# Kernel optimization log

Measured on AMD Instinct MI355X. Metric: run time of the kernel, lower is better.

Reference implementation:

```python
import jax, jax.numpy as jnp
import numpy as np

K = 9  # kernel size == stride, asserted by the module


def setup_inputs() -> dict:
    key = jax.random.key(0)
    k1, k2, k3 = jax.random.split(key, 3)
    x = jax.random.normal(k1, (4, 16, 8192), dtype=jnp.float32)
    W = jax.random.normal(k2, (16, 16, K), dtype=jnp.float32) * 0.1  # conv1d weight [out,in,K]
    b = jax.random.normal(k3, (16,), dtype=jnp.float32) * 0.1       # conv1d bias [out]
    return {"x": x, "W": W, "b": b}


def reference(x, W, b):
    # x: [B, C, N]; sampling_type='all', similarity='Col', aggregation='Col',
    # magnitude='euclidean', no shuffle, no padding, no coordinate encoding.
    B, C, N = x.shape
    # squared euclidean distance matrix [B, N, N]
    ns = jnp.sum(x * x, axis=1)                      # [B, N]
    dot = jnp.einsum('bcn,bcm->bnm', x, x)           # [B, N, N]
    dist = jnp.maximum(ns[:, :, None] + ns[:, None, :] - 2.0 * dot, 0.0)
    # diagonal filled with -0.1 so each token is its own nearest neighbor
    eye = jnp.eye(N, dtype=bool)
    dist = jnp.where(eye[None, :, :], jnp.float32(-0.1), dist)
    # euclidean -> maximum=False -> take K smallest distances
    _, idx = jax.lax.top_k(-dist, K)                 # idx: [B, N, K]
    # gather neighbor features: prime[b, :, n, k] = x[b, :, idx[b, n, k]]
    neigh = jax.vmap(lambda xb, ib: xb[:, ib])(x, idx)   # [B, C, N, K]
    # Conv1d(kernel=K, stride=K, padding=0) over the flattened [B, C, N*K] prime
    # tensor == per-token contraction over (C, K)
    out = jnp.einsum('bcnk,ock->bon', neigh, W) + b[None, :, None]  # [B, out, N]
    return out
```

## Files before the change

### kernel.cpp

```cpp
#include <hip/hip_runtime.h>
#include <hip/hip_bf16.h>
#include <math.h>

#define NB 4
#define NC 16
#define NN 8192
#define NK 9
#define CANDN 128
#define MR (NN / 4)
#define HPAD 129

typedef short s16x8 __attribute__((ext_vector_type(8)));
typedef float f32x4 __attribute__((ext_vector_type(4)));

#define OFF_XS   2097152u
#define OFF_NS   4194304u
#define OFF_NK   4325376u
#define OFF_NBR  4456448u
#define OFF_FLAG 5046272u
#define OFF_CAND 5177344u

__global__ void prep_kernel(const float* __restrict__ x,
                            float* __restrict__ xt,
                            float* __restrict__ ns32,
                            float* __restrict__ nk,
                            unsigned short* __restrict__ xs) {
    int t = blockIdx.x * 256 + threadIdx.x;
    int b = t >> 13, m = t & (NN - 1);
    const float* xb = x + (size_t)b * NC * NN;
    float v[NC];
#pragma unroll
    for (int c = 0; c < NC; ++c) v[c] = xb[(size_t)c * NN + m];
    float s = __fmul_rn(v[0], v[0]);
#pragma unroll
    for (int c = 1; c < NC; ++c) s = __fadd_rn(s, __fmul_rn(v[c], v[c]));
    float* o = xt + (size_t)t * NC;
#pragma unroll
    for (int c = 0; c < NC; ++c) o[c] = v[c];
    ns32[t] = s;
    nk[t] = 128.0f + 0.5f * s;
    unsigned short* xo = xs + (size_t)t * 32;
#pragma unroll
    for (int c = 0; c < NC; ++c) {
        __hip_bfloat16 h = __float2bfloat16(v[c]);
        float hf = __bfloat162float(h);
        __hip_bfloat16 l = __float2bfloat16(v[c] - hf);
        xo[c] = *(unsigned short*)&h;
        xo[16 + c] = *(unsigned short*)&l;
    }
}

__device__ __forceinline__ s16x8 negbf(s16x8 v) {
    s16x8 r;
#pragma unroll
    for (int i = 0; i < 8; ++i) r[i] = (short)(v[i] ^ (short)0x8000);
    return r;
}

__global__ __launch_bounds__(256, 4) void topk_kernel(
        const unsigned short* __restrict__ xs, const float* __restrict__ nk,
        unsigned short* __restrict__ cand, unsigned* __restrict__ flags) {
    __shared__ __align__(16) unsigned hist[32 * HPAD];
    __shared__ __align__(16) unsigned short list[32][CANDN];
    __shared__ unsigned cnt[32];
    __shared__ unsigned Bbin[32];
    const int tid = threadIdx.x;
    const int L = tid & 63;
    const int q = tid >> 6;
    const int b = blockIdx.x >> 8;
    const int n0 = (blockIdx.x & 255) * 32;
    const int lrow = L & 15;
    const int lk = L >> 4;

    {
        for (int i = tid; i < 32 * HPAD; i += 256) hist[i] = 0u;
        unsigned* lp = (unsigned*)&list[0][0];
        for (int i = tid; i < 32 * CANDN / 2; i += 256) lp[i] = 0xFFFFFFFFu;
        if (tid < 32) { cnt[tid] = 0u; Bbin[tid] = 127u; }
    }
    __syncthreads();

    const char* xsb = (const char*)xs + (size_t)b * NN * 64;
    const float* nkb = nk + (size_t)b * NN;
    const char* nkc = (const char*)nkb;

    const int khalf = (lk & 1) * 16;
    const int r0 = n0 + lrow, r1 = n0 + 16 + lrow;
    const s16x8 bhi0 = negbf(*(const s16x8*)(xsb + (size_t)r0 * 64 + khalf));
    const s16x8 blo0 = negbf(*(const s16x8*)(xsb + (size_t)r0 * 64 + 32 + khalf));
    const s16x8 bhi1 = negbf(*(const s16x8*)(xsb + (size_t)r1 * 64 + khalf));
    const s16x8 blo1 = negbf(*(const s16x8*)(xsb + (size_t)r1 * 64 + 32 + khalf));

    const float base8_0 = 8.0f * (256.0f - nkb[r0]);
    const float base8_1 = 8.0f * (256.0f - nkb[r1]);

    const int m0 = q * MR;
    const int voffA0 = (m0 + lrow) * 64 + lk * 16;
    const int voffK0 = (m0 + lk * 4) * 4;

    {
        int vA = voffA0, vK = voffK0;
        for (int t = 0; t < 64; ++t) {
            const s16x8 a = *(const s16x8*)(xsb + vA);
            const f32x4 nkv = *(const f32x4*)(nkc + vK);
            f32x4 acc0 = __builtin_amdgcn_mfma_f32_16x16x32_bf16(a, bhi0, nkv, 0, 0, 0);
            acc0 = __builtin_amdgcn_mfma_f32_16x16x32_bf16(a, blo0, acc0, 0, 0, 0);
            f32x4 acc1 = __builtin_amdgcn_mfma_f32_16x16x32_bf16(a, bhi1, nkv, 0, 0, 0);
            acc1 = __builtin_amdgcn_mfma_f32_16x16x32_bf16(a, blo1, acc1, 0, 0, 0);
#pragma unroll
            for (int r = 0; r < 4; ++r) {
                const float rr = fmaf(acc0[r], 8.0f, -base8_0);
                if (rr < 127.0f) {
                    const unsigned bin = (unsigned)fmaxf(rr, 0.0f);
                    atomicAdd(&hist[lrow * HPAD + bin], 1u);
                }
            }
#pragma unroll
            for (int r = 0; r < 4; ++r) {
                const float rr = fmaf(acc1[r], 8.0f, -base8_1);
                if (rr < 127.0f) {
                    const unsigned bin = (unsigned)fmaxf(rr, 0.0f);
                    atomicAdd(&hist[(16 + lrow) * HPAD + bin], 1u);
                }
            }
            vA += 1024;
            vK += 64;
        }
    }
    __syncthreads();
    if (tid < 32) {
        unsigned cum = 0;
        unsigned Bv = 127u;
        for (int j = 0; j < 127; ++j) {
            cum += hist[tid * HPAD + j];
            if (cum >= 12u) { Bv = (unsigned)j; break; }
        }
        Bbin[tid] = Bv;
    }
    __syncthreads();
    const unsigned B0 = Bbin[lrow], B1 = Bbin[16 + lrow];
    const float thrf0 = (base8_0 + (float)B0 + 1.25f) * 0.125f;
    const float thrf1 = (base8_1 + (float)B1 + 1.25f) * 0.125f;

    {
        int vA = voffA0, vK = voffK0;
        for (int t = 0; t < MR / 16; ++t) {
            const s16x8 a = *(const s16x8*)(xsb + vA);
            const f32x4 nkv = *(const f32x4*)(nkc + vK);
            f32x4 acc0 = __builtin_amdgcn_mfma_f32_16x16x32_bf16(a, bhi0, nkv, 0, 0, 0);
            acc0 = __builtin_amdgcn_mfma_f32_16x16x32_bf16(a, blo0, acc0, 0, 0, 0);
            f32x4 acc1 = __builtin_amdgcn_mfma_f32_16x16x32_bf16(a, bhi1, nkv, 0, 0, 0);
            acc1 = __builtin_amdgcn_mfma_f32_16x16x32_bf16(a, blo1, acc1, 0, 0, 0);
            const float mn0 = fminf(fminf(acc0[0], acc0[1]),
                                    fminf(acc0[2], acc0[3]));
            if (mn0 < thrf0) {
#pragma unroll
                for (int r = 0; r < 4; ++r) {
                    if (acc0[r] < thrf0) {
                        const unsigned m =
                            (unsigned)(m0 + t * 16 + lk * 4 + r);
                        const unsigned idx = atomicAdd(&cnt[lrow], 1u);
                        if (idx < CANDN)
                            list[lrow][idx] = (unsigned short)m;
                    }
                }
            }
            const float mn1 = fminf(fminf(acc1[0], acc1[1]),
                                    fminf(acc1[2], acc1[3]));
            if (mn1 < thrf1) {
#pragma unroll
                for (int r = 0; r < 4; ++r) {
                    if (acc1[r] < thrf1) {
                        const unsigned m =
                            (unsigned)(m0 + t * 16 + lk * 4 + r);
                        const unsigned idx = atomicAdd(&cnt[16 + lrow], 1u);
                        if (idx < CANDN)
                            list[16 + lrow][idx] = (unsigned short)m;
                    }
                }
            }
            vA += 1024;
            vK += 64;
        }
    }
    __syncthreads();

    {
        const int rr = tid >> 3, seg = tid & 7;
        const unsigned grow = (unsigned)(b * NN + n0 + rr);
        const uint4* src =
            (const uint4*)((const char*)&list[0][0] + rr * 256 + seg * 32);
        uint4* dst = (uint4*)((char*)cand + (size_t)grow * 256 + seg * 32);
        dst[0] = src[0];
        dst[1] = src[1];
    }
    if (tid < 32) {
        const bool bad = (cnt[tid] > (unsigned)CANDN) || (Bbin[tid] == 127u);
        flags[b * NN + n0 + tid] = bad ? 0xFFFFFFFFu : cnt[tid];
    }
}

__global__ __launch_bounds__(256) void rerank_kernel(
        const float* __restrict__ xt, const float* __restrict__ ns32,
        const unsigned short* __restrict__ cand,
        const unsigned* __restrict__ flags,
        unsigned short* __restrict__ nbr) {
    __shared__ unsigned long long mk[64][36];
    const int tid = threadIdx.x;
    const int lr = tid >> 2;
    const int j = tid & 3;
    const int row = blockIdx.x * 64 + lr;
    const int b = row >> 13;
    const int n = row & (NN - 1);
    const float* xb = xt + (size_t)b * NN * NC;
    const float* xrow = xb + (size_t)n * NC;
    float xv[NC];
#pragma unroll
    for (int c = 0; c < NC; ++c) xv[c] = xrow[c];
    const float nsn = ns32[row];
    const float* nsb = ns32 + b * NN;

    unsigned long long lst[NK];
#pragma unroll
    for (int i = 0; i < NK; ++i) lst[i] = ~0ULL;

    auto consider = [&](int m) {
        const float* col = xb + (size_t)m * NC;
        float dot = 0.0f;
#pragma unroll
        for (int c = 0; c < NC; ++c)
            dot = fmaf(xv[c], col[c], dot);
        float dist = __fsub_rn(__fadd_rn(nsn, nsb[m]), __fmul_rn(2.0f, dot));
        dist = fmaxf(dist, 0.0f);
        const unsigned k32 = (m == n) ? 0u
                                      : (__float_as_uint(dist) | 0x80000000u);
        unsigned long long key = ((unsigned long long)k32 << 32) | (unsigned)m;
        if (key < lst[NK - 1]) {
#pragma unroll
            for (int i = 0; i < NK; ++i) {
                unsigned long long aa = lst[i];
                bool sm = key < aa;
                unsigned long long lo = sm ? key : aa;
                unsigned long long hi = sm ? aa : key;
                lst[i] = lo;
                key = hi;
            }
        }
    };

    const unsigned nv = flags[row];
    if (nv == 0xFFFFFFFFu) {
        for (int m = j * (NN / 4); m < (j + 1) * (NN / 4); ++m) consider(m);
    } else {
        const unsigned short* cl = cand + (size_t)row * CANDN;
        for (unsigned jj = (unsigned)j; jj < nv; jj += 4) consider(cl[jj]);
    }
#pragma unroll
    for (int i = 0; i < NK; ++i) mk[lr][j * NK + i] = lst[i];
    __syncthreads();
    if (j == 0) {
        unsigned long long fin[NK];
#pragma unroll
        for (int i = 0; i < NK; ++i) fin[i] = ~0ULL;
        for (int s = 0; s < 4 * NK; ++s) {
            unsigned long long key = mk[lr][s];
            if (key < fin[NK - 1]) {
#pragma unroll
                for (int i = 0; i < NK; ++i) {
                    unsigned long long aa = fin[i];
                    bool sm = key < aa;
                    unsigned long long lo = sm ? key : aa;
                    unsigned long long hi = sm ? aa : key;
                    fin[i] = lo;
                    key = hi;
                }
            }
        }
        unsigned short* o = nbr + (size_t)row * NK;
#pragma unroll
        for (int k = 0; k < NK; ++k) o[k] = (unsigned short)(fin[k] & 0xFFFFu);
    }
}

__global__ __launch_bounds__(256) void conv_kernel(
        const float* __restrict__ xt, const unsigned short* __restrict__ nbr,
        const float* __restrict__ W, const float* __restrict__ bias,
        float* __restrict__ out) {
    const int tid = threadIdx.x;
    const int ob = blockIdx.x >> 7;
    const int rb = blockIdx.x & 127;
    const int row = rb * 256 + tid;
    const int b = rb >> 5;
    const int n = row & (NN - 1);
    const float* xb = xt + (size_t)b * NN * NC;
    const float* Wo = W + ob * (NC * NK);
    const unsigned short* nl = nbr + (size_t)row * NK;

    float acc = bias[ob];
    for (int k = 0; k < NK; ++k) {
        const float* col = xb + (size_t)nl[k] * NC;
        float cv[NC];
#pragma unroll
        for (int c = 0; c < NC; ++c) cv[c] = col[c];
#pragma unroll
        for (int c = 0; c < NC; ++c)
            acc = fmaf(Wo[c * NK + k], cv[c], acc);
    }
    out[(size_t)b * NC * NN + (size_t)ob * NN + n] = acc;
}

extern "C" void kernel_launch(void* const* d_in, const int* in_sizes, int n_in,
                              void* d_out, int out_size, void* d_ws, size_t ws_size,
                              hipStream_t stream) {
    const float* x = (const float*)d_in[0];
    const float* W = (const float*)d_in[1];
    const float* bias = (const float*)d_in[2];
    float* out = (float*)d_out;

    char* ws = (char*)d_ws;
    float* xt = (float*)ws;
    unsigned short* xs = (unsigned short*)(ws + OFF_XS);
    float* ns32 = (float*)(ws + OFF_NS);
    float* nk = (float*)(ws + OFF_NK);
    unsigned short* nbr = (unsigned short*)(ws + OFF_NBR);
    unsigned* flags = (unsigned*)(ws + OFF_FLAG);
    unsigned short* cand = (unsigned short*)(ws + OFF_CAND);

    prep_kernel<<<128, 256, 0, stream>>>(x, xt, ns32, nk, xs);
    topk_kernel<<<1024, 256, 0, stream>>>(xs, nk, cand, flags);
    rerank_kernel<<<512, 256, 0, stream>>>(xt, ns32, cand, flags, nbr);
    conv_kernel<<<2048, 256, 0, stream>>>(xt, nbr, W, bias, out);
}
```

Baseline: 186.4 us.

## Split topk candidate scan across two blocks per row tile with per-half thresholds

The topk kernel now runs 2048 blocks, with each block covering half of the key range for its 32 query rows. Each half builds its own coarser 64-bin histogram from a smaller sample, writes up to 64 candidates into its half of the candidate row, and merges its count and bad flag into a packed flags word through atomicOr. The prep kernel zeroes the flags, and rerank reads the two candidate sublists. The aim is more parallelism and occupancy, since shared memory drops and launch bounds rise to 8. The cost is that coarser bins and per-half thresholds may admit more candidates or trigger full-scan fallbacks more often.

```diff
diff --git a/kernel.cpp b/kernel.cpp
--- a/kernel.cpp
+++ b/kernel.cpp
@@ -6,9 +6,9 @@
 #define NC 16
 #define NN 8192
 #define NK 9
-#define CANDN 128
-#define MR (NN / 4)
-#define HPAD 129
+#define HCAP 64
+#define NBIN 64
+#define HPAD 65
 
 typedef short s16x8 __attribute__((ext_vector_type(8)));
 typedef float f32x4 __attribute__((ext_vector_type(4)));
@@ -24,7 +24,8 @@
                             float* __restrict__ xt,
                             float* __restrict__ ns32,
                             float* __restrict__ nk,
-                            unsigned short* __restrict__ xs) {
+                            unsigned short* __restrict__ xs,
+                            unsigned* __restrict__ flags) {
     int t = blockIdx.x * 256 + threadIdx.x;
     int b = t >> 13, m = t & (NN - 1);
     const float* xb = x + (size_t)b * NC * NN;
@@ -39,6 +40,7 @@
     for (int c = 0; c < NC; ++c) o[c] = v[c];
     ns32[t] = s;
     nk[t] = 128.0f + 0.5f * s;
+    flags[t] = 0u;
     unsigned short* xo = xs + (size_t)t * 32;
 #pragma unroll
     for (int c = 0; c < NC; ++c) {
@@ -57,26 +59,29 @@
     return r;
 }
 
-__global__ __launch_bounds__(256, 4) void topk_kernel(
+__global__ __launch_bounds__(256, 8) void topk_kernel(
         const unsigned short* __restrict__ xs, const float* __restrict__ nk,
         unsigned short* __restrict__ cand, unsigned* __restrict__ flags) {
     __shared__ __align__(16) unsigned hist[32 * HPAD];
-    __shared__ __align__(16) unsigned short list[32][CANDN];
+    __shared__ __align__(16) unsigned short list[32][HCAP];
     __shared__ unsigned cnt[32];
     __shared__ unsigned Bbin[32];
     const int tid = threadIdx.x;
     const int L = tid & 63;
-    const int q = tid >> 6;
-    const int b = blockIdx.x >> 8;
-    const int n0 = (blockIdx.x & 255) * 32;
+    const int wq = tid >> 6;
+    const int bid = blockIdx.x;
+    const int b = bid >> 9;
+    const int rem = bid & 511;
+    const int n0 = (rem >> 1) * 32;
+    const int q2 = rem & 1;
     const int lrow = L & 15;
     const int lk = L >> 4;
 
     {
         for (int i = tid; i < 32 * HPAD; i += 256) hist[i] = 0u;
         unsigned* lp = (unsigned*)&list[0][0];
-        for (int i = tid; i < 32 * CANDN / 2; i += 256) lp[i] = 0xFFFFFFFFu;
-        if (tid < 32) { cnt[tid] = 0u; Bbin[tid] = 127u; }
+        for (int i = tid; i < 32 * HCAP / 2; i += 256) lp[i] = 0xFFFFFFFFu;
+        if (tid < 32) { cnt[tid] = 0u; Bbin[tid] = (unsigned)(NBIN - 1); }
     }
     __syncthreads();
 
@@ -91,12 +96,56 @@
     const s16x8 bhi1 = negbf(*(const s16x8*)(xsb + (size_t)r1 * 64 + khalf));
     const s16x8 blo1 = negbf(*(const s16x8*)(xsb + (size_t)r1 * 64 + 32 + khalf));
 
-    const float base8_0 = 8.0f * (256.0f - nkb[r0]);
-    const float base8_1 = 8.0f * (256.0f - nkb[r1]);
-
-    const int m0 = q * MR;
+    const float base4_0 = 4.0f * (256.0f - nkb[r0]);
+    const float base4_1 = 4.0f * (256.0f - nkb[r1]);
+
+    const int m0 = q2 * (NN / 2) + wq * (NN / 8);
     const int voffA0 = (m0 + lrow) * 64 + lk * 16;
     const int voffK0 = (m0 + lk * 4) * 4;
+
+    {
+        int vA = voffA0, vK = voffK0;
+        for (int t = 0; t < 32; ++t) {
+            const s16x8 a = *(const s16x8*)(xsb + vA);
+            const f32x4 nkv = *(const f32x4*)(nkc + vK);
+            f32x4 acc0 = __builtin_amdgcn_mfma_f32_16x16x32_bf16(a, bhi0, nkv, 0, 0, 0);
+            acc0 = __builtin_amdgcn_mfma_f32_16x16x32_bf16(a, blo0, acc0, 0, 0, 0);
+            f32x4 acc1 = __builtin_amdgcn_mfma_f32_16x16x32_bf16(a, bhi1, nkv, 0, 0, 0);
+            acc1 = __builtin_amdgcn_mfma_f32_16x16x32_bf16(a, blo1, acc1, 0, 0, 0);
+#pragma unroll
+            for (int r = 0; r < 4; ++r) {
+                const float rr = fmaf(acc0[r], 4.0f, -base4_0);
+                if (rr < (float)(NBIN - 1)) {
+                    const unsigned bin = (unsigned)fmaxf(rr, 0.0f);
+                    atomicAdd(&hist[lrow * HPAD + bin], 1u);
+                }
+            }
+#pragma unroll
+            for (int r = 0; r < 4; ++r) {
+                const float rr = fmaf(acc1[r], 4.0f, -base4_1);
+                if (rr < (float)(NBIN - 1)) {
+                    const unsigned bin = (unsigned)fmaxf(rr, 0.0f);
+                    atomicAdd(&hist[(16 + lrow) * HPAD + bin], 1u);
+                }
+            }
+            vA += 1024;
+            vK += 64;
+        }
+    }
+    __syncthreads();
+    if (tid < 32) {
+        unsigned cum = 0;
+        unsigned Bv = (unsigned)(NBIN - 1);
+        for (int j = 0; j < NBIN - 1; ++j) {
+            cum += hist[tid * HPAD + j];
+            if (cum >= 12u) { Bv = (unsigned)j; break; }
+        }
+        Bbin[tid] = Bv;
+    }
+    __syncthreads();
+    const unsigned B0 = Bbin[lrow], B1 = Bbin[16 + lrow];
+    const float thrf0 = (base4_0 + (float)B0 + 1.25f) * 0.25f;
+    const float thrf1 = (base4_1 + (float)B1 + 1.25f) * 0.25f;
 
     {
         int vA = voffA0, vK = voffK0;
@@ -107,50 +156,6 @@
             acc0 = __builtin_amdgcn_mfma_f32_16x16x32_bf16(a, blo0, acc0, 0, 0, 0);
             f32x4 acc1 = __builtin_amdgcn_mfma_f32_16x16x32_bf16(a, bhi1, nkv, 0, 0, 0);
             acc1 = __builtin_amdgcn_mfma_f32_16x16x32_bf16(a, blo1, acc1, 0, 0, 0);
-#pragma unroll
-            for (int r = 0; r < 4; ++r) {
-                const float rr = fmaf(acc0[r], 8.0f, -base8_0);
-                if (rr < 127.0f) {
-                    const unsigned bin = (unsigned)fmaxf(rr, 0.0f);
-                    atomicAdd(&hist[lrow * HPAD + bin], 1u);
-                }
-            }
-#pragma unroll
-            for (int r = 0; r < 4; ++r) {
-                const float rr = fmaf(acc1[r], 8.0f, -base8_1);
-                if (rr < 127.0f) {
-                    const unsigned bin = (unsigned)fmaxf(rr, 0.0f);
-                    atomicAdd(&hist[(16 + lrow) * HPAD + bin], 1u);
-                }
-            }
-            vA += 1024;
-            vK += 64;
-        }
-    }
-    __syncthreads();
-    if (tid < 32) {
-        unsigned cum = 0;
-        unsigned Bv = 127u;
-        for (int j = 0; j < 127; ++j) {
-            cum += hist[tid * HPAD + j];
-            if (cum >= 12u) { Bv = (unsigned)j; break; }
-        }
-        Bbin[tid] = Bv;
-    }
-    __syncthreads();
-    const unsigned B0 = Bbin[lrow], B1 = Bbin[16 + lrow];
-    const float thrf0 = (base8_0 + (float)B0 + 1.25f) * 0.125f;
-    const float thrf1 = (base8_1 + (float)B1 + 1.25f) * 0.125f;
-
-    {
-        int vA = voffA0, vK = voffK0;
-        for (int t = 0; t < MR / 16; ++t) {
-            const s16x8 a = *(const s16x8*)(xsb + vA);
-            const f32x4 nkv = *(const f32x4*)(nkc + vK);
-            f32x4 acc0 = __builtin_amdgcn_mfma_f32_16x16x32_bf16(a, bhi0, nkv, 0, 0, 0);
-            acc0 = __builtin_amdgcn_mfma_f32_16x16x32_bf16(a, blo0, acc0, 0, 0, 0);
-            f32x4 acc1 = __builtin_amdgcn_mfma_f32_16x16x32_bf16(a, bhi1, nkv, 0, 0, 0);
-            acc1 = __builtin_amdgcn_mfma_f32_16x16x32_bf16(a, blo1, acc1, 0, 0, 0);
             const float mn0 = fminf(fminf(acc0[0], acc0[1]),
                                     fminf(acc0[2], acc0[3]));
             if (mn0 < thrf0) {
@@ -160,7 +165,7 @@
                         const unsigned m =
                             (unsigned)(m0 + t * 16 + lk * 4 + r);
                         const unsigned idx = atomicAdd(&cnt[lrow], 1u);
-                        if (idx < CANDN)
+                        if (idx < HCAP)
                             list[lrow][idx] = (unsigned short)m;
                     }
                 }
@@ -174,7 +179,7 @@
                         const unsigned m =
                             (unsigned)(m0 + t * 16 + lk * 4 + r);
                         const unsigned idx = atomicAdd(&cnt[16 + lrow], 1u);
-                        if (idx < CANDN)
+                        if (idx < HCAP)
                             list[16 + lrow][idx] = (unsigned short)m;
                     }
                 }
@@ -189,14 +194,18 @@
         const int rr = tid >> 3, seg = tid & 7;
         const unsigned grow = (unsigned)(b * NN + n0 + rr);
         const uint4* src =
-            (const uint4*)((const char*)&list[0][0] + rr * 256 + seg * 32);
-        uint4* dst = (uint4*)((char*)cand + (size_t)grow * 256 + seg * 32);
+            (const uint4*)((const char*)&list[0][0] + rr * 128 + seg * 16);
+        uint4* dst = (uint4*)((char*)cand + (size_t)grow * 256 + q2 * 128 +
+                              seg * 16);
         dst[0] = src[0];
-        dst[1] = src[1];
     }
     if (tid < 32) {
-        const bool bad = (cnt[tid] > (unsigned)CANDN) || (Bbin[tid] == 127u);
-        flags[b * NN + n0 + tid] = bad ? 0xFFFFFFFFu : cnt[tid];
+        const unsigned c = cnt[tid];
+        const bool bad = (c > (unsigned)HCAP) ||
+                         (Bbin[tid] == (unsigned)(NBIN - 1));
+        const unsigned v = ((c > (unsigned)HCAP ? (unsigned)HCAP : c)
+                            << (8 * q2)) | (bad ? 0x80000000u : 0u);
+        atomicOr(&flags[b * NN + n0 + tid], v);
     }
 }
 
@@ -248,12 +257,16 @@
         }
     };
 
-    const unsigned nv = flags[row];
-    if (nv == 0xFFFFFFFFu) {
+    const unsigned f = flags[row];
+    if (f & 0x80000000u) {
         for (int m = j * (NN / 4); m < (j + 1) * (NN / 4); ++m) consider(m);
     } else {
-        const unsigned short* cl = cand + (size_t)row * CANDN;
-        for (unsigned jj = (unsigned)j; jj < nv; jj += 4) consider(cl[jj]);
+        const unsigned nv0 = f & 0xFFu;
+        const unsigned nv1 = (f >> 8) & 0xFFu;
+        const unsigned short* cl = cand + (size_t)row * 128;
+        for (unsigned jj = (unsigned)j; jj < nv0; jj += 4) consider(cl[jj]);
+        for (unsigned jj = (unsigned)j; jj < nv1; jj += 4)
+            consider(cl[HCAP + jj]);
     }
 #pragma unroll
     for (int i = 0; i < NK; ++i) mk[lr][j * NK + i] = lst[i];
@@ -326,8 +339,8 @@
     unsigned* flags = (unsigned*)(ws + OFF_FLAG);
     unsigned short* cand = (unsigned short*)(ws + OFF_CAND);
 
-    prep_kernel<<<128, 256, 0, stream>>>(x, xt, ns32, nk, xs);
-    topk_kernel<<<1024, 256, 0, stream>>>(xs, nk, cand, flags);
+    prep_kernel<<<128, 256, 0, stream>>>(x, xt, ns32, nk, xs, flags);
+    topk_kernel<<<2048, 256, 0, stream>>>(xs, nk, cand, flags);
     rerank_kernel<<<512, 256, 0, stream>>>(xt, ns32, cand, flags, nbr);
     conv_kernel<<<2048, 256, 0, stream>>>(xt, nbr, W, bias, out);
 }
```

Result: slower. 552.1 us (+196.3%).
